# Optimization experiments

Measured on AMD Instinct MI355X. Metric: run time of the kernel, lower is better.

The kernel has to match this reference:

```python
import math
import jax, jax.numpy as jnp
import numpy as np

N_EMBED = 1024
N_HEAD = 16
B, T = 2, 2048


def _gelu_tanh(x):
    # GPT-2 tanh-approx GELU
    c = math.sqrt(2.0 / math.pi)
    return 0.5 * x * (1.0 + jnp.tanh(c * (x + 0.044715 * x * x * x)))


def _layer_norm(x, w, b, eps=1e-5):
    mu = jnp.mean(x, axis=-1, keepdims=True)
    var = jnp.var(x, axis=-1, keepdims=True)
    return (x - mu) * jax.lax.rsqrt(var + eps) * w + b


def setup_inputs() -> dict:
    key = jax.random.key(0)
    ks = jax.random.split(key, 8)
    s = lambda fan_in: 1.0 / math.sqrt(fan_in)
    return {
        "x": jax.random.normal(ks[0], (B, T, N_EMBED), jnp.float32),
        "ln1_w": jnp.ones((N_EMBED,), jnp.float32),
        "ln1_b": jnp.zeros((N_EMBED,), jnp.float32),
        "W_attn": jax.random.normal(ks[1], (N_EMBED, 3 * N_EMBED), jnp.float32) * s(N_EMBED),
        "b_attn": jnp.zeros((3 * N_EMBED,), jnp.float32),
        "W_o": jax.random.normal(ks[2], (N_EMBED, N_EMBED), jnp.float32) * s(N_EMBED),
        "b_o": jnp.zeros((N_EMBED,), jnp.float32),
        "ln2_w": jnp.ones((N_EMBED,), jnp.float32),
        "ln2_b": jnp.zeros((N_EMBED,), jnp.float32),
        "W_fc": jax.random.normal(ks[3], (N_EMBED, 4 * N_EMBED), jnp.float32) * s(N_EMBED),
        "b_fc": jnp.zeros((4 * N_EMBED,), jnp.float32),
        "W_proj": jax.random.normal(ks[4], (4 * N_EMBED, N_EMBED), jnp.float32) * s(4 * N_EMBED),
        "b_proj": jnp.zeros((N_EMBED,), jnp.float32),
    }


def reference(x, ln1_w, ln1_b, W_attn, b_attn, W_o, b_o,
              ln2_w, ln2_b, W_fc, b_fc, W_proj, b_proj):
    Bx, Tx, C = x.shape
    H = N_HEAD
    Dh = C // H

    # --- attention ---
    h = _layer_norm(x, ln1_w, ln1_b)
    qkv = h @ W_attn + b_attn                       # [B,T,3C]
    q, k, v = jnp.split(qkv, 3, axis=-1)
    q = q.reshape(Bx, Tx, H, Dh).transpose(0, 2, 1, 3)   # [B,H,T,Dh]
    k = k.reshape(Bx, Tx, H, Dh).transpose(0, 2, 1, 3)
    v = v.reshape(Bx, Tx, H, Dh).transpose(0, 2, 1, 3)

    attn = jnp.einsum("bhqd,bhkd->bhqk", q, k) * (1.0 / math.sqrt(Dh))
    causal = jnp.tril(jnp.ones((Tx, Tx), dtype=bool))
    attn = jnp.where(causal[None, None], attn, -jnp.inf)
    attn = jax.nn.softmax(attn, axis=-1)
    y = jnp.einsum("bhqk,bhkd->bhqd", attn, v)      # [B,H,T,Dh]
    y = y.transpose(0, 2, 1, 3).reshape(Bx, Tx, C)
    y = y @ W_o + b_o
    x = x + y

    # --- MLP ---
    h = _layer_norm(x, ln2_w, ln2_b)
    h = _gelu_tanh(h @ W_fc + b_fc)
    h = h @ W_proj + b_proj
    return x + h
```

## Files before the change

kernel.cpp:

```cpp
#include <hip/hip_runtime.h>
#include <math.h>

constexpr int TDIM = 2048;
constexpr int BDIM = 2;
constexpr int CDIM = 1024;
constexpr int HEADS = 16;
constexpr int DH = 64;
constexpr int MDIM = BDIM * TDIM;

typedef short bf16x8 __attribute__((ext_vector_type(8)));
typedef float f32x4 __attribute__((ext_vector_type(4)));
typedef float f32x16 __attribute__((ext_vector_type(16)));

__device__ __forceinline__ float b2f(unsigned short u) {
    union { float f; unsigned int i; } v; v.i = ((unsigned int)u) << 16; return v.f;
}
__device__ __forceinline__ unsigned short f2b(float f) {
    union { float f; unsigned int i; } v; v.f = f;
    unsigned int r = (v.i + 0x7FFFu + ((v.i >> 16) & 1u)) >> 16;
    return (unsigned short)r;
}
__device__ __forceinline__ unsigned int cvtpk(float lo, float hi) {
    unsigned int r;
    asm("v_cvt_pk_bf16_f32 %0, %1, %2" : "=v"(r) : "v"(lo), "v"(hi));
    return r;
}
__device__ __forceinline__ float gelu_f(float x) {
    const float c0 = 0.7978845608028654f;
    float x3 = x * x * x;
    float t = tanhf(c0 * (x + 0.044715f * x3));
    return 0.5f * x * (1.0f + t);
}
__device__ __forceinline__ void async_copy16(const void* g, void* l) {
    __builtin_amdgcn_global_load_lds(
        (const __attribute__((address_space(1))) unsigned int*)g,
        (__attribute__((address_space(3))) unsigned int*)l, 16, 0, 0);
}

__global__ __launch_bounds__(256) void transpose_cast(
    const float* __restrict__ W, unsigned short* __restrict__ Wt, int K, int N) {
    __shared__ float tile[32][33];
    int n0 = blockIdx.x * 32, k0 = blockIdx.y * 32;
    int tx = threadIdx.x & 31, ty = threadIdx.x >> 5;
#pragma unroll
    for (int i = 0; i < 32; i += 8)
        tile[ty + i][tx] = W[(size_t)(k0 + ty + i) * N + n0 + tx];
    __syncthreads();
#pragma unroll
    for (int i = 0; i < 32; i += 8)
        Wt[(size_t)(n0 + ty + i) * K + k0 + tx] = f2b(tile[tx][ty + i]);
}

__global__ __launch_bounds__(256) void ln_kernel(
    const float* __restrict__ x, const float* __restrict__ w,
    const float* __restrict__ b, unsigned short* __restrict__ out) {
    int row = blockIdx.x;
    int tid = threadIdx.x;
    const float* xr = x + (size_t)row * CDIM;
    float4 v = *(const float4*)(xr + tid * 4);
    float s  = v.x + v.y + v.z + v.w;
    float ss = v.x * v.x + v.y * v.y + v.z * v.z + v.w * v.w;
#pragma unroll
    for (int off = 32; off >= 1; off >>= 1) {
        s  += __shfl_xor(s, off);
        ss += __shfl_xor(ss, off);
    }
    __shared__ float rs[4], rss[4];
    int wave = tid >> 6;
    if ((tid & 63) == 0) { rs[wave] = s; rss[wave] = ss; }
    __syncthreads();
    s  = rs[0] + rs[1] + rs[2] + rs[3];
    ss = rss[0] + rss[1] + rss[2] + rss[3];
    float mean = s * (1.0f / CDIM);
    float var  = ss * (1.0f / CDIM) - mean * mean;
    float rstd = rsqrtf(var + 1e-5f);
    float4 wv = *(const float4*)(w + tid * 4);
    float4 bv = *(const float4*)(b + tid * 4);
    ushort4 o;
    o.x = f2b((v.x - mean) * rstd * wv.x + bv.x);
    o.y = f2b((v.y - mean) * rstd * wv.y + bv.y);
    o.z = f2b((v.z - mean) * rstd * wv.z + bv.z);
    o.w = f2b((v.w - mean) * rstd * wv.w + bv.w);
    *(ushort4*)(out + (size_t)row * CDIM + tid * 4) = o;
}

template <int MODE, int BN>
__global__ __launch_bounds__(256) void gemm_bf16(
    const unsigned short* __restrict__ A, const unsigned short* __restrict__ Wt,
    const float* __restrict__ bias, const float* __restrict__ res,
    void* __restrict__ Cout, int M, int N, int K) {
    constexpr int JF = BN / 32;
    __shared__ __align__(16) short As[128 * 64];
    __shared__ __align__(16) short Bs[BN * 64];
    const int tid = threadIdx.x;
    const int lane = tid & 63, w = tid >> 6;
    const int wr = w >> 1, wc = w & 1;
    const int row0 = blockIdx.y * 128, col0 = blockIdx.x * BN;

    const int sr = lane >> 3;
    const int sc = 8 * ((lane & 7) ^ sr);
    const unsigned short* gA = A  + (size_t)(row0 + w * 8 + sr) * K + sc;
    const unsigned short* gB = Wt + (size_t)(col0 + w * 8 + sr) * K + sc;
    short* ldsA = As + (w * 8) * 64;
    short* ldsB = Bs + (w * 8) * 64;

    f32x4 acc[4][JF] = {};
    const int h = lane >> 4;
    const int r15 = lane & 15;

    for (int k0 = 0; k0 < K; k0 += 64) {
        __syncthreads();
#pragma unroll
        for (int i = 0; i < 4; ++i)
            async_copy16(gA + (size_t)i * 32 * K + k0, ldsA + i * 32 * 64);
#pragma unroll
        for (int i = 0; i < JF; ++i)
            async_copy16(gB + (size_t)i * 32 * K + k0, ldsB + i * 32 * 64);
        __syncthreads();
#pragma unroll
        for (int ks = 0; ks < 2; ++ks) {
            bf16x8 af[4], bfr[JF];
#pragma unroll
            for (int i = 0; i < 4; ++i) {
                int ra = wr * 64 + i * 16 + r15;
                int offa = ra * 128 + ((ks * 64 + h * 16) ^ ((ra & 7) << 4));
                af[i] = *(const bf16x8*)((const char*)As + offa);
            }
#pragma unroll
            for (int j = 0; j < JF; ++j) {
                int rb = wc * (BN / 2) + j * 16 + r15;
                int offb = rb * 128 + ((ks * 64 + h * 16) ^ ((rb & 7) << 4));
                bfr[j] = *(const bf16x8*)((const char*)Bs + offb);
            }
#pragma unroll
            for (int i = 0; i < 4; ++i)
#pragma unroll
                for (int j = 0; j < JF; ++j)
                    acc[i][j] = __builtin_amdgcn_mfma_f32_16x16x32_bf16(
                        af[i], bfr[j], acc[i][j], 0, 0, 0);
        }
    }

#pragma unroll
    for (int i = 0; i < 4; ++i) {
#pragma unroll
        for (int j = 0; j < JF; ++j) {
            int c = col0 + wc * (BN / 2) + j * 16 + r15;
            float bv = bias[c];
#pragma unroll
            for (int q = 0; q < 4; ++q) {
                int rr = row0 + wr * 64 + i * 16 + h * 4 + q;
                float v = acc[i][j][q] + bv;
                if (MODE == 2) v = gelu_f(v);
                if (MODE == 1) v += res[(size_t)rr * N + c];
                if (MODE == 1) ((float*)Cout)[(size_t)rr * N + c] = v;
                else ((unsigned short*)Cout)[(size_t)rr * N + c] = f2b(v);
            }
        }
    }
}

__global__ __launch_bounds__(512, 4) void attn_mfma(
    const unsigned short* __restrict__ qkv, unsigned short* __restrict__ y) {
    const int bh = blockIdx.x;
    const int b = bh >> 4, hh = bh & 15;
    const int by = blockIdx.y;
    const int qy = (by < 8) ? (15 - by) : (by - 8);
    const int q0 = qy * 128;
    const int tid = threadIdx.x;
    const int lane = tid & 63, w = tid >> 6;
    const int p = w & 3, half = w >> 2;
    const int hi = lane >> 5, q31 = lane & 31;

    const float SC  = 0.1803368801111244f;
    const float THR = 44.0f;

    __shared__ __align__(16) char smem[36864];
    float (*Os)[68] = (float (*)[68])smem;
    float* mlm = (float*)(smem + 34816);
    float* mll = (float*)(smem + 34816 + 1024);

    const size_t base = (size_t)b * TDIM * (3 * CDIM);
    const unsigned short* qb = qkv + base + hh * DH;
    const unsigned short* kb = qkv + base + CDIM + hh * DH;
    const unsigned short* vb = qkv + base + 2 * CDIM + hh * DH;

    const int gq = q0 + p * 32 + q31;
    const int qmin_w = q0 + p * 32;
    const int qmax_w = qmin_w + 31;

    bf16x8 qf[4];
#pragma unroll
    for (int ks = 0; ks < 4; ++ks)
        qf[ks] = *(const bf16x8*)(qb + (size_t)gq * (3 * CDIM) + ks * 16 + hi * 8);

    const int sr = lane >> 3;
    const int scK = 8 * ((lane & 7) ^ sr);
    const int rV = tid >> 3;
    const int dblk = (tid & 7) * 8;

    f32x16 oacc[2] = {};
    float m = -1e30f, l = 0.f;
    bf16x8 vreg;

    const int NT = 2 * qy + 2;

    {
        short* Ks0 = (short*)smem;
        int rowbase = w * 8;
        async_copy16(kb + (size_t)(rowbase + sr) * (3 * CDIM) + scK, Ks0 + rowbase * 64);
        vreg = *(const bf16x8*)(vb + (size_t)rV * (3 * CDIM) + dblk);
        char* Vt0 = smem + 16384;
#pragma unroll
        for (int j = 0; j < 8; ++j) {
            int d = dblk + j;
            int swz = ((d ^ (d >> 3)) & 7) << 4;
            *(short*)(Vt0 + d * 128 + ((2 * rV) ^ swz)) = vreg[j];
        }
    }
    __syncthreads();

    for (int kt = 0; kt < NT; ++kt) {
        const int c = kt & 1;
        const char* Ksc = smem + c * 8192;
        const char* Vtc = smem + 16384 + c * 8192;
        const bool pre = (kt + 1 < NT);

        if (pre) {
            const int kv1 = (kt + 1) * 64;
            short* Ksn = (short*)(smem + (c ^ 1) * 8192);
            int rowbase = w * 8;
            async_copy16(kb + (size_t)(kv1 + rowbase + sr) * (3 * CDIM) + scK,
                         Ksn + rowbase * 64);
            vreg = *(const bf16x8*)(vb + (size_t)(kv1 + rV) * (3 * CDIM) + dblk);
        }

        const int kvs = kt * 64 + half * 32;
        if (kvs <= qmax_w) {
            f32x16 sacc = {};
            __builtin_amdgcn_s_setprio(1);
#pragma unroll
            for (int ks = 0; ks < 4; ++ks) {
                int row = half * 32 + q31;
                int off = row * 128 + ((32 * ks + 16 * hi) ^ ((row & 7) << 4));
                bf16x8 kf = *(const bf16x8*)(Ksc + off);
                sacc = __builtin_amdgcn_mfma_f32_32x32x16_bf16(kf, qf[ks], sacc, 0, 0, 0);
            }
            __builtin_amdgcn_s_setprio(0);

            float p_[16];
            if (kvs + 31 > qmin_w) {
#pragma unroll
                for (int r = 0; r < 16; ++r) {
                    int kvg = kvs + (r & 3) + 8 * (r >> 2) + 4 * hi;
                    p_[r] = (kvg > gq) ? -1e30f : sacc[r];
                }
            } else {
#pragma unroll
                for (int r = 0; r < 16; ++r) p_[r] = sacc[r];
            }

            float t8[8];
#pragma unroll
            for (int r = 0; r < 8; ++r) t8[r] = fmaxf(p_[r], p_[r + 8]);
#pragma unroll
            for (int r = 0; r < 4; ++r) t8[r] = fmaxf(t8[r], t8[r + 4]);
            float pm = fmaxf(fmaxf(t8[0], t8[1]), fmaxf(t8[2], t8[3]));
            pm = fmaxf(pm, __shfl_xor(pm, 32));

            if (!__all(pm <= m + THR)) {
                float mnew = fmaxf(m, pm);
                float sf = exp2f((m - mnew) * SC);
                m = mnew;
                l *= sf;
                oacc[0] *= sf;
                oacc[1] *= sf;
            }
            float mc = m * SC;
#pragma unroll
            for (int r = 0; r < 16; ++r) p_[r] = exp2f(fmaf(p_[r], SC, -mc));
#pragma unroll
            for (int r = 0; r < 8; ++r) t8[r] = p_[r] + p_[r + 8];
#pragma unroll
            for (int r = 0; r < 4; ++r) t8[r] = t8[r] + t8[r + 4];
            float rsum = (t8[0] + t8[1]) + (t8[2] + t8[3]);
            rsum += __shfl_xor(rsum, 32);
            l += rsum;

            bf16x8 pa[2];
#pragma unroll
            for (int k2 = 0; k2 < 2; ++k2) {
                unsigned int A0 = cvtpk(p_[8 * k2 + 0], p_[8 * k2 + 1]);
                unsigned int A1 = cvtpk(p_[8 * k2 + 2], p_[8 * k2 + 3]);
                unsigned int B0 = cvtpk(p_[8 * k2 + 4], p_[8 * k2 + 5]);
                unsigned int B1 = cvtpk(p_[8 * k2 + 6], p_[8 * k2 + 7]);
                unsigned int sA0 = __shfl_xor((int)A0, 32);
                unsigned int sA1 = __shfl_xor((int)A1, 32);
                unsigned int sB0 = __shfl_xor((int)B0, 32);
                unsigned int sB1 = __shfl_xor((int)B1, 32);
                union { int i[4]; bf16x8 h; } u;
                u.i[0] = hi ? (int)sB0 : (int)A0;
                u.i[1] = hi ? (int)sB1 : (int)A1;
                u.i[2] = hi ? (int)B0 : (int)sA0;
                u.i[3] = hi ? (int)B1 : (int)sA1;
                pa[k2] = u.h;
            }

            __builtin_amdgcn_s_setprio(1);
#pragma unroll
            for (int j2 = 0; j2 < 2; ++j2) {
                int row = 32 * j2 + q31;
                int swz = ((row ^ (row >> 3)) & 7) << 4;
#pragma unroll
                for (int k2 = 0; k2 < 2; ++k2) {
                    int off = row * 128 + ((64 * half + 32 * k2 + 16 * hi) ^ swz);
                    bf16x8 vf = *(const bf16x8*)(Vtc + off);
                    oacc[j2] = __builtin_amdgcn_mfma_f32_32x32x16_bf16(vf, pa[k2], oacc[j2], 0, 0, 0);
                }
            }
            __builtin_amdgcn_s_setprio(0);
        }

        if (pre) {
            char* Vtn = smem + 16384 + (c ^ 1) * 8192;
#pragma unroll
            for (int j = 0; j < 8; ++j) {
                int d = dblk + j;
                int swz = ((d ^ (d >> 3)) & 7) << 4;
                *(short*)(Vtn + d * 128 + ((2 * rV) ^ swz)) = vreg[j];
            }
        }
        __syncthreads();
    }

    mlm[(half * 4 + p) * 32 + q31] = m;
    mll[(half * 4 + p) * 32 + q31] = l;
    __syncthreads();
    float mo = mlm[((half ^ 1) * 4 + p) * 32 + q31];
    float lo = mll[((half ^ 1) * 4 + p) * 32 + q31];
    float M  = fmaxf(m, mo);
    float sf  = exp2f((m - M) * SC);
    float sfo = exp2f((mo - M) * SC);
    float invl = 1.0f / (l * sf + lo * sfo);

    if (half == 1) {
#pragma unroll
        for (int j2 = 0; j2 < 2; ++j2)
#pragma unroll
            for (int g = 0; g < 4; ++g) {
                float4 v4 = make_float4(oacc[j2][4 * g + 0] * sf, oacc[j2][4 * g + 1] * sf,
                                        oacc[j2][4 * g + 2] * sf, oacc[j2][4 * g + 3] * sf);
                *(float4*)&Os[p * 32 + q31][32 * j2 + 8 * g + 4 * hi] = v4;
            }
    }
    __syncthreads();
    if (half == 0) {
#pragma unroll
        for (int j2 = 0; j2 < 2; ++j2)
#pragma unroll
            for (int g = 0; g < 4; ++g) {
                float4 t = *(const float4*)&Os[p * 32 + q31][32 * j2 + 8 * g + 4 * hi];
                float4 v4;
                v4.x = (oacc[j2][4 * g + 0] * sf + t.x) * invl;
                v4.y = (oacc[j2][4 * g + 1] * sf + t.y) * invl;
                v4.z = (oacc[j2][4 * g + 2] * sf + t.z) * invl;
                v4.w = (oacc[j2][4 * g + 3] * sf + t.w) * invl;
                *(float4*)&Os[p * 32 + q31][32 * j2 + 8 * g + 4 * hi] = v4;
            }
    }
    __syncthreads();

    const int r0 = tid >> 4;
    const int c4 = (tid & 15) * 4;
#pragma unroll
    for (int pass = 0; pass < 4; ++pass) {
        int row = pass * 32 + r0;
        float4 v = *(const float4*)&Os[row][c4];
        ushort4 o;
        o.x = f2b(v.x); o.y = f2b(v.y); o.z = f2b(v.z); o.w = f2b(v.w);
        *(ushort4*)(y + (size_t)(b * TDIM + q0 + row) * CDIM + hh * DH + c4) = o;
    }
}

extern "C" void kernel_launch(void* const* d_in, const int* in_sizes, int n_in,
                              void* d_out, int out_size, void* d_ws, size_t ws_size,
                              hipStream_t stream) {
    const float* x      = (const float*)d_in[0];
    const float* ln1_w  = (const float*)d_in[1];
    const float* ln1_b  = (const float*)d_in[2];
    const float* W_attn = (const float*)d_in[3];
    const float* b_attn = (const float*)d_in[4];
    const float* W_o    = (const float*)d_in[5];
    const float* b_o    = (const float*)d_in[6];
    const float* ln2_w  = (const float*)d_in[7];
    const float* ln2_b  = (const float*)d_in[8];
    const float* W_fc   = (const float*)d_in[9];
    const float* b_fc   = (const float*)d_in[10];
    const float* W_proj = (const float*)d_in[11];
    const float* b_proj = (const float*)d_in[12];
    float* out = (float*)d_out;

    char* ws = (char*)d_ws;
    const size_t MB = 1024 * 1024;
    unsigned short* h_bf    = (unsigned short*)(ws);
    unsigned short* big     = (unsigned short*)(ws + 8 * MB);
    unsigned short* Wt_attn = (unsigned short*)(ws + 40 * MB);
    unsigned short* Wt_o    = (unsigned short*)(ws + 46 * MB);
    unsigned short* Wt_fc   = (unsigned short*)(ws + 48 * MB);
    unsigned short* Wt_proj = (unsigned short*)(ws + 56 * MB);
    float* x1 = out;

    hipLaunchKernelGGL(transpose_cast, dim3(96, 32),  dim3(256), 0, stream, W_attn, Wt_attn, CDIM, 3 * CDIM);
    hipLaunchKernelGGL(transpose_cast, dim3(32, 32),  dim3(256), 0, stream, W_o,    Wt_o,    CDIM, CDIM);
    hipLaunchKernelGGL(transpose_cast, dim3(128, 32), dim3(256), 0, stream, W_fc,   Wt_fc,   CDIM, 4 * CDIM);
    hipLaunchKernelGGL(transpose_cast, dim3(32, 128), dim3(256), 0, stream, W_proj, Wt_proj, 4 * CDIM, CDIM);

    hipLaunchKernelGGL(ln_kernel, dim3(MDIM), dim3(256), 0, stream, x, ln1_w, ln1_b, h_bf);
    hipLaunchKernelGGL((gemm_bf16<0, 128>), dim3(3 * CDIM / 128, MDIM / 128), dim3(256), 0,
                       stream, h_bf, Wt_attn, b_attn, nullptr, big, MDIM, 3 * CDIM, CDIM);
    hipLaunchKernelGGL(attn_mfma, dim3(BDIM * HEADS, TDIM / 128), dim3(512), 0, stream,
                       big, h_bf);
    hipLaunchKernelGGL((gemm_bf16<1, 64>), dim3(CDIM / 64, MDIM / 128), dim3(256), 0,
                       stream, h_bf, Wt_o, b_o, x, x1, MDIM, CDIM, CDIM);
    hipLaunchKernelGGL(ln_kernel, dim3(MDIM), dim3(256), 0, stream, x1, ln2_w, ln2_b, h_bf);
    hipLaunchKernelGGL((gemm_bf16<2, 128>), dim3(4 * CDIM / 128, MDIM / 128), dim3(256), 0,
                       stream, h_bf, Wt_fc, b_fc, nullptr, big, MDIM, 4 * CDIM, CDIM);
    hipLaunchKernelGGL((gemm_bf16<1, 64>), dim3(CDIM / 64, MDIM / 128), dim3(256), 0,
                       stream, big, Wt_proj, b_proj, x1, out, MDIM, CDIM, 4 * CDIM);
}
```

Measured before the change: 272.8 us.

## Double-buffer GEMM LDS tiles with async prefetch and cheaper GELU

The bf16 GEMM now uses two LDS buffers per operand. It issues the global-to-LDS loads for the next K tile before computing on the current one, with an explicit vmcnt wait and barriers, so load latency overlaps with MFMA work. GELU is rewritten as x/(1+exp2(z)), which is algebraically the same as the tanh form and avoids tanhf. Doubling the LDS use may reduce occupancy, and the hand-written waitcnt counts must match the number of loads issued.

Measured after the change: 241.9 us. 11.3% less time.

```diff
diff --git a/kernel.cpp b/kernel.cpp
--- a/kernel.cpp
+++ b/kernel.cpp
@@ -26,10 +26,8 @@
     return r;
 }
 __device__ __forceinline__ float gelu_f(float x) {
-    const float c0 = 0.7978845608028654f;
-    float x3 = x * x * x;
-    float t = tanhf(c0 * (x + 0.044715f * x3));
-    return 0.5f * x * (1.0f + t);
+    float z = -2.3022077f * (x + 0.044715f * x * x * x);
+    return x / (1.0f + exp2f(z));
 }
 __device__ __forceinline__ void async_copy16(const void* g, void* l) {
     __builtin_amdgcn_global_load_lds(
@@ -90,8 +88,9 @@
     const float* __restrict__ bias, const float* __restrict__ res,
     void* __restrict__ Cout, int M, int N, int K) {
     constexpr int JF = BN / 32;
-    __shared__ __align__(16) short As[128 * 64];
-    __shared__ __align__(16) short Bs[BN * 64];
+    constexpr int INF = 4 + JF;
+    __shared__ __align__(16) short As[2][128 * 64];
+    __shared__ __align__(16) short Bs[2][BN * 64];
     const int tid = threadIdx.x;
     const int lane = tid & 63, w = tid >> 6;
     const int wr = w >> 1, wc = w & 1;
@@ -101,22 +100,36 @@
     const int sc = 8 * ((lane & 7) ^ sr);
     const unsigned short* gA = A  + (size_t)(row0 + w * 8 + sr) * K + sc;
     const unsigned short* gB = Wt + (size_t)(col0 + w * 8 + sr) * K + sc;
-    short* ldsA = As + (w * 8) * 64;
-    short* ldsB = Bs + (w * 8) * 64;
 
     f32x4 acc[4][JF] = {};
     const int h = lane >> 4;
     const int r15 = lane & 15;
-
-    for (int k0 = 0; k0 < K; k0 += 64) {
-        __syncthreads();
-#pragma unroll
-        for (int i = 0; i < 4; ++i)
-            async_copy16(gA + (size_t)i * 32 * K + k0, ldsA + i * 32 * 64);
-#pragma unroll
-        for (int i = 0; i < JF; ++i)
-            async_copy16(gB + (size_t)i * 32 * K + k0, ldsB + i * 32 * 64);
-        __syncthreads();
+    const int nt = K >> 6;
+
+#pragma unroll
+    for (int i = 0; i < 4; ++i)
+        async_copy16(gA + (size_t)i * 32 * K, &As[0][(w * 8 + i * 32) * 64]);
+#pragma unroll
+    for (int i = 0; i < JF; ++i)
+        async_copy16(gB + (size_t)i * 32 * K, &Bs[0][(w * 8 + i * 32) * 64]);
+
+    for (int t = 0; t < nt; ++t) {
+        const int c = t & 1;
+        if (t + 1 < nt) {
+            const int k1 = (t + 1) << 6;
+#pragma unroll
+            for (int i = 0; i < 4; ++i)
+                async_copy16(gA + (size_t)i * 32 * K + k1, &As[c ^ 1][(w * 8 + i * 32) * 64]);
+#pragma unroll
+            for (int i = 0; i < JF; ++i)
+                async_copy16(gB + (size_t)i * 32 * K + k1, &Bs[c ^ 1][(w * 8 + i * 32) * 64]);
+            asm volatile("s_waitcnt vmcnt(%0)" :: "n"(INF) : "memory");
+        } else {
+            asm volatile("s_waitcnt vmcnt(0)" ::: "memory");
+        }
+        __builtin_amdgcn_s_barrier();
+        asm volatile("" ::: "memory");
+
 #pragma unroll
         for (int ks = 0; ks < 2; ++ks) {
             bf16x8 af[4], bfr[JF];
@@ -124,13 +137,13 @@
             for (int i = 0; i < 4; ++i) {
                 int ra = wr * 64 + i * 16 + r15;
                 int offa = ra * 128 + ((ks * 64 + h * 16) ^ ((ra & 7) << 4));
-                af[i] = *(const bf16x8*)((const char*)As + offa);
+                af[i] = *(const bf16x8*)((const char*)As[c] + offa);
             }
 #pragma unroll
             for (int j = 0; j < JF; ++j) {
                 int rb = wc * (BN / 2) + j * 16 + r15;
                 int offb = rb * 128 + ((ks * 64 + h * 16) ^ ((rb & 7) << 4));
-                bfr[j] = *(const bf16x8*)((const char*)Bs + offb);
+                bfr[j] = *(const bf16x8*)((const char*)Bs[c] + offb);
             }
 #pragma unroll
             for (int i = 0; i < 4; ++i)
@@ -139,6 +152,8 @@
                     acc[i][j] = __builtin_amdgcn_mfma_f32_16x16x32_bf16(
                         af[i], bfr[j], acc[i][j], 0, 0, 0);
         }
+        asm volatile("" ::: "memory");
+        __builtin_amdgcn_s_barrier();
     }
 
 #pragma unroll
```
